# Kernel optimization log

Measured on AMD Instinct MI355X. Metric: run time of the kernel, lower is better.

The kernel has to match this reference:

```python
import jax, jax.numpy as jnp
import numpy as np

B, SQ, SK, D = 4, 2048, 2048, 1024


def setup_inputs() -> dict:
    key = jax.random.key(0)
    ks = jax.random.split(key, 8)
    s = 1.0 / np.sqrt(D)
    return {
        "input_seq": jax.random.normal(ks[0], (B, SQ, D), jnp.float32),
        "condition_seq": jax.random.normal(ks[1], (B, SK, D), jnp.float32),
        "Wq": jax.random.normal(ks[2], (D, D), jnp.float32) * s,
        "bq": jnp.zeros((D,), jnp.float32),
        "Wk": jax.random.normal(ks[3], (D, D), jnp.float32) * s,
        "bk": jnp.zeros((D,), jnp.float32),
        "Wv": jax.random.normal(ks[4], (D, D), jnp.float32) * s,
        "bv": jnp.zeros((D,), jnp.float32),
    }


def reference(input_seq, condition_seq, Wq, bq, Wk, bk, Wv, bv):
    # Linear projections (torch Linear: x @ W.T + b)
    q = jnp.einsum("bsd,ed->bse", input_seq, Wq) + bq        # [B,SQ,D]
    k = jnp.einsum("btd,ed->bte", condition_seq, Wk) + bk    # [B,SK,D]
    v = jnp.einsum("btd,ed->bte", condition_seq, Wv) + bv    # [B,SK,D]
    # NOTE: original module omits the 1/sqrt(d) scaling — kept faithful.
    scores = jnp.einsum("bse,bte->bst", q, k)                # [B,SQ,SK]
    attn = jax.nn.softmax(scores, axis=-1)
    attended = jnp.einsum("bst,bte->bse", attn, v)           # [B,SQ,D]
    return attended
```

## Files before the change

kernel.cpp:

```cpp
#include <hip/hip_runtime.h>

using f32x4  = __attribute__((ext_vector_type(4))) float;
using bf16x8 = __attribute__((ext_vector_type(8))) __bf16;
using f16x8  = __attribute__((ext_vector_type(8))) _Float16;
using u16x4  = __attribute__((ext_vector_type(4))) unsigned short;
using u16x8  = __attribute__((ext_vector_type(8))) unsigned short;

constexpr int Bb = 4, SQn = 2048, SKn = 2048, Dd = 1024;

__device__ __forceinline__ unsigned fbitsu(float x){ union{float f;unsigned u;}c; c.f=x; return c.u; }
__device__ __forceinline__ float ubitsf(unsigned u){ union{unsigned u;float f;}c; c.u=u; return c.f; }
__device__ __forceinline__ unsigned short hi_trunc(float x){ return (unsigned short)(fbitsu(x)>>16); }
__device__ __forceinline__ unsigned short hi_rne(float x){ unsigned u=fbitsu(x); return (unsigned short)((u + 0x7FFFu + ((u>>16)&1u))>>16); }
__device__ __forceinline__ float from_hi(unsigned short h){ return ubitsf(((unsigned)h)<<16); }
__device__ __forceinline__ unsigned short h_rne(float x){ _Float16 h = (_Float16)x; return __builtin_bit_cast(unsigned short, h); }
__device__ __forceinline__ float h2f(unsigned short u){ return (float)__builtin_bit_cast(_Float16, u); }

template<int DT> __device__ __forceinline__ unsigned short cvt_rne(float x){ return DT ? h_rne(x) : hi_rne(x); }
template<int DT> __device__ __forceinline__ float cvt_f(unsigned short u){ return DT ? h2f(u) : from_hi(u); }

__device__ __forceinline__ f32x4 mfma_bf16(bf16x8 a, bf16x8 b, f32x4 c){
    return __builtin_amdgcn_mfma_f32_16x16x32_bf16(a, b, c, 0, 0, 0);
}
__device__ __forceinline__ f32x4 mfma_f16(u16x8 a, u16x8 b, f32x4 c){
    return __builtin_amdgcn_mfma_f32_16x16x32_f16(
        __builtin_bit_cast(f16x8, a), __builtin_bit_cast(f16x8, b), c, 0, 0, 0);
}
template<int DT>
__device__ __forceinline__ f32x4 mfma_u16(u16x8 a, u16x8 b, f32x4 c){
    if constexpr (DT) return mfma_f16(a, b, c);
    else return __builtin_amdgcn_mfma_f32_16x16x32_bf16(
        __builtin_bit_cast(bf16x8, a), __builtin_bit_cast(bf16x8, b), c, 0, 0, 0);
}

__device__ __forceinline__ void gload16(const void* g, void* l){
    __builtin_amdgcn_global_load_lds(
        (const __attribute__((address_space(1))) unsigned int*)g,
        (__attribute__((address_space(3))) unsigned int*)l, 16, 0, 0);
}

__device__ __forceinline__ void xcd_swz(int& bx, int& by){
    const int nx = gridDim.x, nwg = nx * gridDim.y;
    int l = by * nx + bx;
    l = (l & 7) * (nwg >> 3) + (l >> 3);
    bx = l % nx; by = l / nx;
}

__global__ __launch_bounds__(256)
void split2(const float* __restrict__ x, const float* __restrict__ c,
            unsigned short* __restrict__ xh, unsigned short* __restrict__ xl,
            unsigned short* __restrict__ ch, unsigned short* __restrict__ cl,
            int n4)
{
    const int stride = gridDim.x * 256;
    for (int i = blockIdx.x * 256 + threadIdx.x; i < 2 * n4; i += stride) {
        const bool second = (i >= n4);
        const int j = second ? i - n4 : i;
        const float* in = second ? c : x;
        unsigned short* hi = second ? ch : xh;
        unsigned short* lo = second ? cl : xl;
        float a[4]; *(float4*)a = *(const float4*)(in + (size_t)j * 4);
        u16x4 h, l;
#pragma unroll
        for (int r = 0; r < 4; ++r) {
            h[r] = h_rne(a[r]);
            l[r] = h_rne(a[r] - h2f(h[r]));
        }
        *(u16x4*)&hi[(size_t)j * 4] = h;
        *(u16x4*)&lo[(size_t)j * 4] = l;
    }
}

__global__ __launch_bounds__(256)
void cvtW(const float* __restrict__ Wq, const float* __restrict__ Wk,
          const float* __restrict__ Wv,
          unsigned short* __restrict__ oq, unsigned short* __restrict__ ok,
          unsigned short* __restrict__ ov, int n4)
{
    const int stride = gridDim.x * 256;
    for (int i = blockIdx.x * 256 + threadIdx.x; i < 3 * n4; i += stride) {
        const float* src; unsigned short* dst; int j = i;
        if (j < n4)          { src = Wq; dst = oq; }
        else if (j < 2*n4)   { src = Wk; dst = ok; j -= n4; }
        else                 { src = Wv; dst = ov; j -= 2*n4; }
        float a[4]; *(float4*)a = *(const float4*)(src + (size_t)j * 4);
        u16x4 h;
#pragma unroll
        for (int r = 0; r < 4; ++r) h[r] = h_rne(a[r]);
        *(u16x4*)&dst[(size_t)j * 4] = h;
    }
}

template<int TERMS, int BM_, int BN_, int KS, int EPI, int DT>
__global__ __launch_bounds__(256, 2)
void gemm_tile(const unsigned short* __restrict__ Ahg, const unsigned short* __restrict__ Alg,
               const unsigned short* __restrict__ Bhg, const unsigned short* __restrict__ Blg,
               const float* __restrict__ bias,
               void* __restrict__ O0v, void* __restrict__ O1v,
               int M, int N, int K, long aBS, long bBS, long oBS)
{
    constexpr int CA = BM_ / 16;
    constexpr int CB = BN_ / 16;
    constexpr int AI = BM_ / 32;
    constexpr int BJ = BN_ / 32;
    static_assert(CA % 4 == 0 && CB % 4 == 0, "chunks divisible by 4 waves");

    __shared__ __align__(16) unsigned short Ash[KS][BM_*32], Bsh[KS][BN_*32];
    __shared__ __align__(16) unsigned short Asl[TERMS>=2?KS:1][TERMS>=2?BM_*32:8];
    __shared__ __align__(16) unsigned short Bsl[TERMS==3?KS:1][TERMS==3?BN_*32:8];

    const int z = blockIdx.z;
    Ahg += (size_t)z * aBS;
    Bhg += (size_t)z * bBS;
    if (TERMS >= 2) Alg += (size_t)z * aBS;
    if (TERMS == 3) Blg += (size_t)z * bBS;

    int bx = blockIdx.x, by = blockIdx.y;
    xcd_swz(bx, by);

    const int tid = threadIdx.x, lane = tid & 63, w = tid >> 6;
    const int wr = (w >> 1) * (BM_/2), wc = (w & 1) * (BN_/2);
    const int lr = lane & 15, lg = lane >> 4;
    const int m0 = by * BM_, n0 = bx * BN_;
    const int rowc = lane >> 2;
    const int colb = (lane & 3) << 4;
    const size_t rsBy = (size_t)K * 2;

    f32x4 acc[AI][BJ] = {};

    for (int k0 = 0; k0 < K; k0 += KS*32) {
#pragma unroll
        for (int s = 0; s < KS; ++s) {
#pragma unroll
            for (int c4 = 0; c4 < CA/4; ++c4) {
                const int c = c4*4 + w;
                const size_t go = (size_t)(m0 + c*16 + rowc) * rsBy + (size_t)(k0 + s*32)*2 + colb;
                gload16((const char*)Ahg + go, (char*)&Ash[s][0] + c*1024);
                if (TERMS >= 2) gload16((const char*)Alg + go, (char*)&Asl[s][0] + c*1024);
            }
#pragma unroll
            for (int c4 = 0; c4 < CB/4; ++c4) {
                const int c = c4*4 + w;
                const size_t go = (size_t)(n0 + c*16 + rowc) * rsBy + (size_t)(k0 + s*32)*2 + colb;
                gload16((const char*)Bhg + go, (char*)&Bsh[s][0] + c*1024);
                if (TERMS == 3) gload16((const char*)Blg + go, (char*)&Bsl[s][0] + c*1024);
            }
        }
        __syncthreads();

#pragma unroll
        for (int kk = 0; kk < KS; ++kk) {
            u16x8 ah[AI], bh[BJ];
#pragma unroll
            for (int i = 0; i < AI; ++i) ah[i] = *(const u16x8*)&Ash[kk][(wr + i*16 + lr)*32 + lg*8];
#pragma unroll
            for (int j = 0; j < BJ; ++j) bh[j] = *(const u16x8*)&Bsh[kk][(wc + j*16 + lr)*32 + lg*8];
            if (TERMS == 3) {
                u16x8 al[AI], bl[BJ];
#pragma unroll
                for (int i = 0; i < AI; ++i) al[i] = *(const u16x8*)&Asl[kk][(wr + i*16 + lr)*32 + lg*8];
#pragma unroll
                for (int j = 0; j < BJ; ++j) bl[j] = *(const u16x8*)&Bsl[kk][(wc + j*16 + lr)*32 + lg*8];
#pragma unroll
                for (int i = 0; i < AI; ++i)
#pragma unroll
                    for (int j = 0; j < BJ; ++j) {
                        acc[i][j] = mfma_u16<DT>(ah[i], bh[j], acc[i][j]);
                        acc[i][j] = mfma_u16<DT>(ah[i], bl[j], acc[i][j]);
                        acc[i][j] = mfma_u16<DT>(al[i], bh[j], acc[i][j]);
                    }
            } else if (TERMS == 2) {
                u16x8 al[AI];
#pragma unroll
                for (int i = 0; i < AI; ++i) al[i] = *(const u16x8*)&Asl[kk][(wr + i*16 + lr)*32 + lg*8];
#pragma unroll
                for (int i = 0; i < AI; ++i)
#pragma unroll
                    for (int j = 0; j < BJ; ++j) {
                        acc[i][j] = mfma_u16<DT>(ah[i], bh[j], acc[i][j]);
                        acc[i][j] = mfma_u16<DT>(al[i], bh[j], acc[i][j]);
                    }
            } else {
#pragma unroll
                for (int i = 0; i < AI; ++i)
#pragma unroll
                    for (int j = 0; j < BJ; ++j)
                        acc[i][j] = mfma_u16<DT>(ah[i], bh[j], acc[i][j]);
            }
        }
        __syncthreads();
    }

    if (EPI == 0) {
        float* C = (float*)O0v + (size_t)z * oBS;
#pragma unroll
        for (int j = 0; j < BJ; ++j) {
            const int col = n0 + wc + j*16 + lr;
#pragma unroll
            for (int i = 0; i < AI; ++i)
#pragma unroll
                for (int r = 0; r < 4; ++r)
                    C[(size_t)(m0 + wr + i*16 + lg*4 + r) * N + col] = acc[i][j][r];
        }
    } else {
        unsigned short* Chi = (unsigned short*)O0v + (size_t)z * oBS;
        unsigned short* Clo = (unsigned short*)O1v + (size_t)z * oBS;
#pragma unroll
        for (int j = 0; j < BJ; ++j) {
            const int col = n0 + wc + j*16 + lr;
            const float bc = (EPI == 2) ? bias[col] : 0.f;
#pragma unroll
            for (int i = 0; i < AI; ++i)
#pragma unroll
                for (int r = 0; r < 4; ++r) {
                    const size_t idx = (size_t)(m0 + wr + i*16 + lg*4 + r) * N + col;
                    const float v = acc[i][j][r] + bc;
                    const unsigned short h = cvt_rne<DT>(v);
                    Chi[idx] = h;
                    Clo[idx] = cvt_rne<DT>(v - cvt_f<DT>(h));
                }
        }
    }
}

__global__ __launch_bounds__(256, 2)
void gemm_kv(const unsigned short* __restrict__ Ahg, const unsigned short* __restrict__ Alg,
             const unsigned short* __restrict__ Wk16, const unsigned short* __restrict__ Wv16,
             const float* __restrict__ bk, const float* __restrict__ bv,
             unsigned short* __restrict__ Kh, unsigned short* __restrict__ Vt,
             int M, int N, int K)
{
    constexpr int BM_ = 128, BN_ = 128, BK_ = 32;
    __shared__ __align__(16) unsigned short Ash[BM_*BK_], Asl[BM_*BK_];
    __shared__ __align__(16) unsigned short Bks[BN_*BK_], Bvs[BN_*BK_];

    int bx = blockIdx.x, by = blockIdx.y;
    xcd_swz(bx, by);

    const int tid = threadIdx.x, lane = tid & 63, w = tid >> 6;
    const int wr = (w >> 1) * 64, wc = (w & 1) * 64;
    const int lr = lane & 15, lg = lane >> 4;
    const int m0 = by * BM_, n0 = bx * BN_;
    const int rowc = lane >> 2;
    const int colb = (lane & 3) << 4;
    const size_t rsBy = (size_t)K * 2;

    f32x4 acck[4][4] = {}, accv[4][4] = {};

    for (int k0 = 0; k0 < K; k0 += BK_) {
#pragma unroll
        for (int c4 = 0; c4 < 2; ++c4) {
            const int c = c4*4 + w;
            const size_t goA = (size_t)(m0 + c*16 + rowc) * rsBy + (size_t)k0*2 + colb;
            gload16((const char*)Ahg + goA, (char*)Ash + c*1024);
            gload16((const char*)Alg + goA, (char*)Asl + c*1024);
            const size_t goB = (size_t)(n0 + c*16 + rowc) * rsBy + (size_t)k0*2 + colb;
            gload16((const char*)Wk16 + goB, (char*)Bks + c*1024);
            gload16((const char*)Wv16 + goB, (char*)Bvs + c*1024);
        }
        __syncthreads();

        u16x8 ah[4], al[4], bf[4];
#pragma unroll
        for (int i = 0; i < 4; ++i) {
            ah[i] = *(const u16x8*)&Ash[(wr + i*16 + lr)*BK_ + lg*8];
            al[i] = *(const u16x8*)&Asl[(wr + i*16 + lr)*BK_ + lg*8];
        }
#pragma unroll
        for (int j = 0; j < 4; ++j) bf[j] = *(const u16x8*)&Bks[(wc + j*16 + lr)*BK_ + lg*8];
#pragma unroll
        for (int i = 0; i < 4; ++i)
#pragma unroll
            for (int j = 0; j < 4; ++j) {
                acck[i][j] = mfma_f16(ah[i], bf[j], acck[i][j]);
                acck[i][j] = mfma_f16(al[i], bf[j], acck[i][j]);
            }
#pragma unroll
        for (int j = 0; j < 4; ++j) bf[j] = *(const u16x8*)&Bvs[(wc + j*16 + lr)*BK_ + lg*8];
#pragma unroll
        for (int i = 0; i < 4; ++i)
#pragma unroll
            for (int j = 0; j < 4; ++j) {
                accv[i][j] = mfma_f16(ah[i], bf[j], accv[i][j]);
                accv[i][j] = mfma_f16(al[i], bf[j], accv[i][j]);
            }
        __syncthreads();
    }

#pragma unroll
    for (int j = 0; j < 4; ++j) {
        const int col = n0 + wc + j*16 + lr;
        const float bck = bk[col], bcv = bv[col];
#pragma unroll
        for (int i = 0; i < 4; ++i) {
            const int row0 = m0 + wr + i*16 + lg*4;
#pragma unroll
            for (int r = 0; r < 4; ++r)
                Kh[(size_t)(row0 + r)*N + col] = h_rne(acck[i][j][r] + bck);
            const int b = row0 >> 11, t0 = row0 & 2047;
            u16x4 pk;
#pragma unroll
            for (int r = 0; r < 4; ++r) pk[r] = h_rne(accv[i][j][r] + bcv);
            *(u16x4*)&Vt[(((size_t)b*Dd + col) << 11) + t0] = pk;
        }
    }
}

template<int TERMS, int EPI>
__global__ __launch_bounds__(256, 2)
void gemm_proj(const float* __restrict__ A, const float* __restrict__ Bm,
               const float* __restrict__ bias,
               unsigned short* __restrict__ O0, unsigned short* __restrict__ O1,
               int M, int N, int K)
{
    constexpr int BM_ = 128, BN_ = 64, BK_ = 32;
    __shared__ __align__(16) unsigned short Ash[BM_*BK_], Bsh[BN_*BK_];
    __shared__ __align__(16) unsigned short Asl[TERMS==3?BM_*BK_:8], Bsl[TERMS==3?BN_*BK_:8];

    const int tid = threadIdx.x, lane = tid & 63, w = tid >> 6;
    const int wr = (w >> 1) * 64, wc = (w & 1) * 32;
    const int lr = lane & 15, lg = lane >> 4;
    const int m0 = blockIdx.y * BM_, n0 = blockIdx.x * BN_;

    f32x4 acc[4][2] = {};

    for (int k0 = 0; k0 < K; k0 += BK_) {
        float4 av[4], bv[2];
#pragma unroll
        for (int u = 0; u < 4; ++u) {
            const int f = u*256 + tid;
            av[u] = *(const float4*)(A + (size_t)(m0 + (f >> 3))*K + k0 + ((f & 7) << 2));
        }
#pragma unroll
        for (int u = 0; u < 2; ++u) {
            const int f = u*256 + tid;
            bv[u] = *(const float4*)(Bm + (size_t)(n0 + (f >> 3))*K + k0 + ((f & 7) << 2));
        }
        __syncthreads();
#pragma unroll
        for (int u = 0; u < 4; ++u) {
            const int f = u*256 + tid;
            const int row = f >> 3, ko = (f & 7) << 2;
            float a4[4]; *(float4*)a4 = av[u];
            u16x4 ah;
            if (TERMS == 3) {
                u16x4 al;
#pragma unroll
                for (int j = 0; j < 4; ++j) { ah[j] = hi_trunc(a4[j]); al[j] = hi_trunc(a4[j] - from_hi(ah[j])); }
                *(u16x4*)&Asl[row*BK_ + ko] = al;
            } else {
#pragma unroll
                for (int j = 0; j < 4; ++j) ah[j] = hi_rne(a4[j]);
            }
            *(u16x4*)&Ash[row*BK_ + ko] = ah;
        }
#pragma unroll
        for (int u = 0; u < 2; ++u) {
            const int f = u*256 + tid;
            const int row = f >> 3, ko = (f & 7) << 2;
            float b4[4]; *(float4*)b4 = bv[u];
            u16x4 bh;
            if (TERMS == 3) {
                u16x4 bl;
#pragma unroll
                for (int j = 0; j < 4; ++j) { bh[j] = hi_trunc(b4[j]); bl[j] = hi_trunc(b4[j] - from_hi(bh[j])); }
                *(u16x4*)&Bsl[row*BK_ + ko] = bl;
            } else {
#pragma unroll
                for (int j = 0; j < 4; ++j) bh[j] = hi_rne(b4[j]);
            }
            *(u16x4*)&Bsh[row*BK_ + ko] = bh;
        }
        __syncthreads();

        bf16x8 ah[4], bh[2];
#pragma unroll
        for (int i = 0; i < 4; ++i) ah[i] = *(const bf16x8*)&Ash[(wr + i*16 + lr)*BK_ + lg*8];
#pragma unroll
        for (int j = 0; j < 2; ++j) bh[j] = *(const bf16x8*)&Bsh[(wc + j*16 + lr)*BK_ + lg*8];
        if (TERMS == 3) {
            bf16x8 al[4], bl[2];
#pragma unroll
            for (int i = 0; i < 4; ++i) al[i] = *(const bf16x8*)&Asl[(wr + i*16 + lr)*BK_ + lg*8];
#pragma unroll
            for (int j = 0; j < 2; ++j) bl[j] = *(const bf16x8*)&Bsl[(wc + j*16 + lr)*BK_ + lg*8];
#pragma unroll
            for (int i = 0; i < 4; ++i)
#pragma unroll
                for (int j = 0; j < 2; ++j) {
                    acc[i][j] = mfma_bf16(ah[i], bh[j], acc[i][j]);
                    acc[i][j] = mfma_bf16(ah[i], bl[j], acc[i][j]);
                    acc[i][j] = mfma_bf16(al[i], bh[j], acc[i][j]);
                }
        } else {
#pragma unroll
            for (int i = 0; i < 4; ++i)
#pragma unroll
                for (int j = 0; j < 2; ++j)
                    acc[i][j] = mfma_bf16(ah[i], bh[j], acc[i][j]);
        }
        __syncthreads();
    }

#pragma unroll
    for (int j = 0; j < 2; ++j) {
        const int col = n0 + wc + j*16 + lr;
        const float bc = bias[col];
#pragma unroll
        for (int i = 0; i < 4; ++i) {
            if (EPI == 0) {
#pragma unroll
                for (int r = 0; r < 4; ++r) {
                    const int row = m0 + wr + i*16 + lg*4 + r;
                    const float v = acc[i][j][r] + bc;
                    const unsigned short h = h_rne(v);
                    O0[(size_t)row*N + col] = h;
                    O1[(size_t)row*N + col] = h_rne(v - h2f(h));
                }
            } else if (EPI == 2) {
#pragma unroll
                for (int r = 0; r < 4; ++r) {
                    const int row = m0 + wr + i*16 + lg*4 + r;
                    O0[(size_t)row*N + col] = h_rne(acc[i][j][r] + bc);
                }
            } else {
                const int row0 = m0 + wr + i*16 + lg*4;
                const int b = row0 >> 11, t0 = row0 & 2047;
                u16x4 pk;
#pragma unroll
                for (int r = 0; r < 4; ++r) pk[r] = h_rne(acc[i][j][r] + bc);
                *(u16x4*)&O0[(((size_t)b*Dd + col) << 11) + t0] = pk;
            }
        }
    }
}

__global__ __launch_bounds__(256)
void softmax_sp(unsigned short* __restrict__ Shi, const unsigned short* __restrict__ Slo)
{
    const int tid = threadIdx.x;
    unsigned short* ph = Shi + (size_t)blockIdx.x * SKn;
    const unsigned short* pl = Slo + (size_t)blockIdx.x * SKn;
    __shared__ float red[8];

    u16x4 h0 = *(const u16x4*)&ph[tid*4];
    u16x4 h1 = *(const u16x4*)&ph[1024 + tid*4];
    u16x4 l0 = *(const u16x4*)&pl[tid*4];
    u16x4 l1 = *(const u16x4*)&pl[1024 + tid*4];
    float v[8];
#pragma unroll
    for (int r = 0; r < 4; ++r) {
        v[r]   = h2f(h0[r]) + h2f(l0[r]);
        v[4+r] = h2f(h1[r]) + h2f(l1[r]);
    }
    float m = v[0];
#pragma unroll
    for (int r = 1; r < 8; ++r) m = fmaxf(m, v[r]);
#pragma unroll
    for (int o2 = 32; o2 > 0; o2 >>= 1) m = fmaxf(m, __shfl_down(m, o2));
    if ((tid & 63) == 0) red[tid >> 6] = m;
    __syncthreads();
    m = fmaxf(fmaxf(red[0],red[1]), fmaxf(red[2],red[3]));

    float e[8], s = 0.f;
#pragma unroll
    for (int r = 0; r < 8; ++r) { e[r] = __expf(v[r] - m); s += e[r]; }
#pragma unroll
    for (int o2 = 32; o2 > 0; o2 >>= 1) s += __shfl_down(s, o2);
    if ((tid & 63) == 0) red[4 + (tid >> 6)] = s;
    __syncthreads();
    const float inv = 1.f / ((red[4]+red[5])+(red[6]+red[7]));

    u16x4 p0, p1;
#pragma unroll
    for (int r = 0; r < 4; ++r) { p0[r] = h_rne(e[r]*inv); p1[r] = h_rne(e[4+r]*inv); }
    *(u16x4*)&ph[tid*4] = p0;
    *(u16x4*)&ph[1024 + tid*4] = p1;
}

extern "C" void kernel_launch(void* const* d_in, const int* in_sizes, int n_in,
                              void* d_out, int out_size, void* d_ws, size_t ws_size,
                              hipStream_t stream)
{
    const float* x  = (const float*)d_in[0];
    const float* c  = (const float*)d_in[1];
    const float* Wq = (const float*)d_in[2];
    const float* bq = (const float*)d_in[3];
    const float* Wk = (const float*)d_in[4];
    const float* bk = (const float*)d_in[5];
    const float* Wv = (const float*)d_in[6];
    const float* bv = (const float*)d_in[7];
    float* out = (float*)d_out;

    const size_t nQ = (size_t)Bb * SQn * Dd;
    const size_t sE = (size_t)SQn * SKn;
    const size_t nW = (size_t)Dd * Dd;
    unsigned short* Qh = (unsigned short*)d_ws;
    unsigned short* Ql = Qh + nQ;
    unsigned short* Kh = Ql + nQ;
    unsigned short* Kl = Kh + nQ;
    unsigned short* Vt = Kl + nQ;
    unsigned short* Shi = Vt + nQ;
    unsigned short* Slo = Shi + (size_t)Bb * sE;

    unsigned short* Wq16 = Kl;
    unsigned short* Wk16 = Kl + nW;
    unsigned short* Wv16 = Kl + 2*nW;

    unsigned short* xh = Shi;
    unsigned short* xl = Shi + nQ;
    unsigned short* ch = Slo;
    unsigned short* cl = Slo + nQ;

    const size_t needB = (size_t)(Shi - Qh) * 2 + (size_t)Bb * sE * 2 * 2;
    const bool batched = ws_size >= needB;

    const dim3 blk(256);

    if (batched) {
        split2<<<dim3(4096), blk, 0, stream>>>(x, c, xh, xl, ch, cl, (int)(nQ/4));
        cvtW<<<dim3(1024), blk, 0, stream>>>(Wq, Wk, Wv, Wq16, Wk16, Wv16, (int)(nW/4));

        gemm_tile<2,128,128,2,2,1><<<dim3(Dd/128, (Bb*SQn)/128), blk, 0, stream>>>(
            xh, xl, Wq16, nullptr, bq, Qh, Ql, Bb*SQn, Dd, Dd, 0, 0, 0);
        gemm_kv<<<dim3(Dd/128, (Bb*SKn)/128), blk, 0, stream>>>(
            ch, cl, Wk16, Wv16, bk, bv, Kh, Vt, Bb*SKn, Dd, Dd);

        gemm_tile<2,128,128,1,1,1><<<dim3(SKn/128, SQn/128, Bb), blk, 0, stream>>>(
            Qh, Ql, Kh, nullptr, nullptr, Shi, Slo, SQn, SKn, Dd,
            (long)SQn*Dd, (long)SKn*Dd, (long)sE);
        softmax_sp<<<dim3(Bb*SQn), blk, 0, stream>>>(Shi, Slo);
        gemm_tile<1,128,128,2,0,1><<<dim3(Dd/128, SQn/128, Bb), blk, 0, stream>>>(
            Shi, nullptr, Vt, nullptr, nullptr, out, nullptr, SQn, Dd, SKn,
            (long)sE, (long)Dd*SKn, (long)SQn*Dd);
    } else {
        unsigned short* ShiF = Shi;
        unsigned short* SloF = Shi + sE;
        gemm_proj<3,0><<<dim3(Dd/64, (Bb*SQn)/128), blk, 0, stream>>>(x, Wq, bq, Qh, Ql, Bb*SQn, Dd, Dd);
        gemm_proj<3,2><<<dim3(Dd/64, (Bb*SKn)/128), blk, 0, stream>>>(c, Wk, bk, Kh, nullptr, Bb*SKn, Dd, Dd);
        gemm_proj<1,1><<<dim3(Dd/64, (Bb*SKn)/128), blk, 0, stream>>>(c, Wv, bv, Vt, nullptr, Bb*SKn, Dd, Dd);
        for (int b = 0; b < Bb; ++b) {
            const size_t qoff = (size_t)b * SQn * Dd;
            const size_t koff = (size_t)b * SKn * Dd;
            gemm_tile<2,128,64,1,1,1><<<dim3(SKn/64, SQn/128, 1), blk, 0, stream>>>(
                Qh+qoff, Ql+qoff, Kh+koff, nullptr, nullptr, ShiF, SloF, SQn, SKn, Dd, 0, 0, 0);
            softmax_sp<<<dim3(SQn), blk, 0, stream>>>(ShiF, SloF);
            gemm_tile<1,64,64,1,0,1><<<dim3(Dd/64, SQn/64, 1), blk, 0, stream>>>(
                ShiF, nullptr, Vt+(size_t)b*Dd*SKn, nullptr, nullptr, out+qoff, nullptr,
                SQn, Dd, SKn, 0, 0, 0);
        }
    }
}
```

Baseline: 276.5 us.

## Merge input conversion kernels, add double-buffered score GEMM, vectorize softmax IO

Fuses the activation split and weight conversion into one prep kernel to save a launch. Replaces the generic score GEMM with a dedicated kernel that double-buffers LDS tiles through direct global-to-LDS loads and overlaps the next stage's loads with the current MFMA work. Softmax now loads and stores 8 halves per thread in a single vector access. The new GEMM epilogue writes scalar shorts per element, which may cost some store efficiency.

```diff
diff --git a/kernel.cpp b/kernel.cpp
--- a/kernel.cpp
+++ b/kernel.cpp
@@ -47,47 +47,132 @@
 }
 
 __global__ __launch_bounds__(256)
-void split2(const float* __restrict__ x, const float* __restrict__ c,
-            unsigned short* __restrict__ xh, unsigned short* __restrict__ xl,
-            unsigned short* __restrict__ ch, unsigned short* __restrict__ cl,
-            int n4)
+void prep(const float* __restrict__ x, const float* __restrict__ c,
+          const float* __restrict__ Wq, const float* __restrict__ Wk,
+          const float* __restrict__ Wv,
+          unsigned short* __restrict__ xh, unsigned short* __restrict__ xl,
+          unsigned short* __restrict__ ch, unsigned short* __restrict__ cl,
+          unsigned short* __restrict__ oq, unsigned short* __restrict__ ok,
+          unsigned short* __restrict__ ov,
+          int n4, int nw4)
 {
+    const int total = 2*n4 + 3*nw4;
     const int stride = gridDim.x * 256;
-    for (int i = blockIdx.x * 256 + threadIdx.x; i < 2 * n4; i += stride) {
-        const bool second = (i >= n4);
-        const int j = second ? i - n4 : i;
-        const float* in = second ? c : x;
-        unsigned short* hi = second ? ch : xh;
-        unsigned short* lo = second ? cl : xl;
-        float a[4]; *(float4*)a = *(const float4*)(in + (size_t)j * 4);
-        u16x4 h, l;
-#pragma unroll
-        for (int r = 0; r < 4; ++r) {
-            h[r] = h_rne(a[r]);
-            l[r] = h_rne(a[r] - h2f(h[r]));
-        }
-        *(u16x4*)&hi[(size_t)j * 4] = h;
-        *(u16x4*)&lo[(size_t)j * 4] = l;
-    }
-}
-
-__global__ __launch_bounds__(256)
-void cvtW(const float* __restrict__ Wq, const float* __restrict__ Wk,
-          const float* __restrict__ Wv,
-          unsigned short* __restrict__ oq, unsigned short* __restrict__ ok,
-          unsigned short* __restrict__ ov, int n4)
+    for (int i = blockIdx.x * 256 + threadIdx.x; i < total; i += stride) {
+        if (i < 2*n4) {
+            const bool second = (i >= n4);
+            const int j = second ? i - n4 : i;
+            const float* in = second ? c : x;
+            unsigned short* hi = second ? ch : xh;
+            unsigned short* lo = second ? cl : xl;
+            float a[4]; *(float4*)a = *(const float4*)(in + (size_t)j * 4);
+            u16x4 h, l;
+#pragma unroll
+            for (int r = 0; r < 4; ++r) {
+                h[r] = h_rne(a[r]);
+                l[r] = h_rne(a[r] - h2f(h[r]));
+            }
+            *(u16x4*)&hi[(size_t)j * 4] = h;
+            *(u16x4*)&lo[(size_t)j * 4] = l;
+        } else {
+            int j = i - 2*n4;
+            const float* src; unsigned short* dst;
+            if (j < nw4)          { src = Wq; dst = oq; }
+            else if (j < 2*nw4)   { src = Wk; dst = ok; j -= nw4; }
+            else                  { src = Wv; dst = ov; j -= 2*nw4; }
+            float a[4]; *(float4*)a = *(const float4*)(src + (size_t)j * 4);
+            u16x4 h;
+#pragma unroll
+            for (int r = 0; r < 4; ++r) h[r] = h_rne(a[r]);
+            *(u16x4*)&dst[(size_t)j * 4] = h;
+        }
+    }
+}
+
+__global__ __launch_bounds__(256, 2)
+void gemm_sc(const unsigned short* __restrict__ Qhg, const unsigned short* __restrict__ Qlg,
+             const unsigned short* __restrict__ Khg,
+             unsigned short* __restrict__ Shi, unsigned short* __restrict__ Slo,
+             int M, int N, int K, long aBS, long bBS, long oBS)
 {
-    const int stride = gridDim.x * 256;
-    for (int i = blockIdx.x * 256 + threadIdx.x; i < 3 * n4; i += stride) {
-        const float* src; unsigned short* dst; int j = i;
-        if (j < n4)          { src = Wq; dst = oq; }
-        else if (j < 2*n4)   { src = Wk; dst = ok; j -= n4; }
-        else                 { src = Wv; dst = ov; j -= 2*n4; }
-        float a[4]; *(float4*)a = *(const float4*)(src + (size_t)j * 4);
-        u16x4 h;
-#pragma unroll
-        for (int r = 0; r < 4; ++r) h[r] = h_rne(a[r]);
-        *(u16x4*)&dst[(size_t)j * 4] = h;
+    constexpr int BM_ = 128, BN_ = 128;
+    __shared__ __align__(16) unsigned short Ash[2][BM_*32], Bsh[2][BN_*32];
+
+    const int z = blockIdx.z;
+    Qhg += (size_t)z * aBS;
+    Qlg += (size_t)z * aBS;
+    Khg += (size_t)z * bBS;
+
+    int bx = blockIdx.x, by = blockIdx.y;
+    xcd_swz(bx, by);
+
+    const int tid = threadIdx.x, lane = tid & 63, w = tid >> 6;
+    const int wr = (w >> 1) * 64, wc = (w & 1) * 64;
+    const int lr = lane & 15, lg = lane >> 4;
+    const int m0 = by * BM_, n0 = bx * BN_;
+    const int rowc = lane >> 2;
+    const int colb = (lane & 3) << 4;
+    const size_t rsBy = (size_t)K * 2;
+
+    auto stage = [&](int t, int buf){
+        const int k0 = t * 32;
+        const bool lo = (k0 >= K);
+        const unsigned short* Ap = lo ? Qlg : Qhg;
+        const int km = lo ? k0 - K : k0;
+#pragma unroll
+        for (int c4 = 0; c4 < 2; ++c4) {
+            const int c = c4*4 + w;
+            const size_t goA = (size_t)(m0 + c*16 + rowc) * rsBy + (size_t)km*2 + colb;
+            gload16((const char*)Ap + goA, (char*)&Ash[buf][0] + c*1024);
+            const size_t goB = (size_t)(n0 + c*16 + rowc) * rsBy + (size_t)km*2 + colb;
+            gload16((const char*)Khg + goB, (char*)&Bsh[buf][0] + c*1024);
+        }
+    };
+
+    f32x4 acc[4][4] = {};
+    const int nt = (2 * K) / 32;
+
+    stage(0, 0);
+    for (int t = 0; t < nt; ++t) {
+        const int cur = t & 1;
+        if (t + 1 < nt) {
+            stage(t + 1, cur ^ 1);
+            asm volatile("s_waitcnt vmcnt(4)" ::: "memory");
+        } else {
+            asm volatile("s_waitcnt vmcnt(0)" ::: "memory");
+        }
+        __builtin_amdgcn_sched_barrier(0);
+        __builtin_amdgcn_s_barrier();
+
+        u16x8 af[4], bf[4];
+#pragma unroll
+        for (int i = 0; i < 4; ++i) af[i] = *(const u16x8*)&Ash[cur][(wr + i*16 + lr)*32 + lg*8];
+#pragma unroll
+        for (int j = 0; j < 4; ++j) bf[j] = *(const u16x8*)&Bsh[cur][(wc + j*16 + lr)*32 + lg*8];
+#pragma unroll
+        for (int i = 0; i < 4; ++i)
+#pragma unroll
+            for (int j = 0; j < 4; ++j)
+                acc[i][j] = mfma_f16(af[i], bf[j], acc[i][j]);
+
+        __builtin_amdgcn_s_barrier();
+    }
+
+    unsigned short* Chi = Shi + (size_t)z * oBS;
+    unsigned short* Clo = Slo + (size_t)z * oBS;
+#pragma unroll
+    for (int j = 0; j < 4; ++j) {
+        const int col = n0 + wc + j*16 + lr;
+#pragma unroll
+        for (int i = 0; i < 4; ++i)
+#pragma unroll
+            for (int r = 0; r < 4; ++r) {
+                const size_t idx = (size_t)(m0 + wr + i*16 + lg*4 + r) * N + col;
+                const float v = acc[i][j][r];
+                const unsigned short h = h_rne(v);
+                Chi[idx] = h;
+                Clo[idx] = h_rne(v - h2f(h));
+            }
     }
 }
 
@@ -443,16 +528,12 @@
     const unsigned short* pl = Slo + (size_t)blockIdx.x * SKn;
     __shared__ float red[8];
 
-    u16x4 h0 = *(const u16x4*)&ph[tid*4];
-    u16x4 h1 = *(const u16x4*)&ph[1024 + tid*4];
-    u16x4 l0 = *(const u16x4*)&pl[tid*4];
-    u16x4 l1 = *(const u16x4*)&pl[1024 + tid*4];
+    u16x8 h8 = *(const u16x8*)&ph[tid*8];
+    u16x8 l8 = *(const u16x8*)&pl[tid*8];
     float v[8];
 #pragma unroll
-    for (int r = 0; r < 4; ++r) {
-        v[r]   = h2f(h0[r]) + h2f(l0[r]);
-        v[4+r] = h2f(h1[r]) + h2f(l1[r]);
-    }
+    for (int r = 0; r < 8; ++r) v[r] = h2f(h8[r]) + h2f(l8[r]);
+
     float m = v[0];
 #pragma unroll
     for (int r = 1; r < 8; ++r) m = fmaxf(m, v[r]);
@@ -471,11 +552,10 @@
     __syncthreads();
     const float inv = 1.f / ((red[4]+red[5])+(red[6]+red[7]));
 
-    u16x4 p0, p1;
-#pragma unroll
-    for (int r = 0; r < 4; ++r) { p0[r] = h_rne(e[r]*inv); p1[r] = h_rne(e[4+r]*inv); }
-    *(u16x4*)&ph[tid*4] = p0;
-    *(u16x4*)&ph[1024 + tid*4] = p1;
+    u16x8 p8;
+#pragma unroll
+    for (int r = 0; r < 8; ++r) p8[r] = h_rne(e[r]*inv);
+    *(u16x8*)&ph[tid*8] = p8;
 }
 
 extern "C" void kernel_launch(void* const* d_in, const int* in_sizes, int n_in,
@@ -518,16 +598,17 @@
     const dim3 blk(256);
 
     if (batched) {
-        split2<<<dim3(4096), blk, 0, stream>>>(x, c, xh, xl, ch, cl, (int)(nQ/4));
-        cvtW<<<dim3(1024), blk, 0, stream>>>(Wq, Wk, Wv, Wq16, Wk16, Wv16, (int)(nW/4));
+        prep<<<dim3(4096), blk, 0, stream>>>(x, c, Wq, Wk, Wv,
+                                             xh, xl, ch, cl, Wq16, Wk16, Wv16,
+                                             (int)(nQ/4), (int)(nW/4));
 
         gemm_tile<2,128,128,2,2,1><<<dim3(Dd/128, (Bb*SQn)/128), blk, 0, stream>>>(
             xh, xl, Wq16, nullptr, bq, Qh, Ql, Bb*SQn, Dd, Dd, 0, 0, 0);
         gemm_kv<<<dim3(Dd/128, (Bb*SKn)/128), blk, 0, stream>>>(
             ch, cl, Wk16, Wv16, bk, bv, Kh, Vt, Bb*SKn, Dd, Dd);
 
-        gemm_tile<2,128,128,1,1,1><<<dim3(SKn/128, SQn/128, Bb), blk, 0, stream>>>(
-            Qh, Ql, Kh, nullptr, nullptr, Shi, Slo, SQn, SKn, Dd,
+        gemm_sc<<<dim3(SKn/128, SQn/128, Bb), blk, 0, stream>>>(
+            Qh, Ql, Kh, Shi, Slo, SQn, SKn, Dd,
             (long)SQn*Dd, (long)SKn*Dd, (long)sE);
         softmax_sp<<<dim3(Bb*SQn), blk, 0, stream>>>(Shi, Slo);
         gemm_tile<1,128,128,2,0,1><<<dim3(Dd/128, SQn/128, Bb), blk, 0, stream>>>(
```

New measurement: 285.3 us. +3.2%, slower.
